# Performance work log

Measured on AMD Instinct MI355X. Metric: run time of the kernel, lower is better.

Reference implementation:

```python
import jax, jax.numpy as jnp
import numpy as np
import math

NUM_HEADS = 12
POS_BND = 16                 # patch_num
RPE_NUM = 2 * POS_BND + 1    # 33
LOGIT_SCALE_MAX = math.log(1.0 / 0.01)
EPS_NORM = 1e-12


def setup_inputs() -> dict:
    key = jax.random.key(0)
    ks = jax.random.split(key, 8)
    L, N, C = 257, 32, 768   # L = 16*16 patches + 1 CLS
    H, W = 16, 16
    x = jax.random.normal(ks[0], (L, N, C), dtype=jnp.float32)
    depth = jax.random.uniform(ks[1], (N, 1, H, W), dtype=jnp.float32)
    in_proj_w = jax.random.normal(ks[2], (3 * C, C), dtype=jnp.float32) * 0.02
    in_proj_b = jnp.zeros((3 * C,), dtype=jnp.float32)
    out_proj_w = jax.random.normal(ks[3], (C, C), dtype=jnp.float32) * 0.02
    out_proj_b = jnp.zeros((C,), dtype=jnp.float32)
    rpe_table = jax.random.normal(ks[4], (3 * RPE_NUM, NUM_HEADS), dtype=jnp.float32) * 0.02
    logit_scale = jnp.log(10.0) * jnp.ones((NUM_HEADS, 1, 1), dtype=jnp.float32)
    return {
        "x": x, "depth": depth,
        "in_proj_w": in_proj_w, "in_proj_b": in_proj_b,
        "out_proj_w": out_proj_w, "out_proj_b": out_proj_b,
        "rpe_table": rpe_table, "logit_scale": logit_scale,
    }


def _rpe_bias(depth, rpe_table):
    # depth: (B, 1, H, W) -> bias (B*num_heads, H*W, H*W)
    d = depth[:, 0]                              # (B, H, W)
    B, H, W = d.shape
    ii, jj = jnp.meshgrid(jnp.arange(H), jnp.arange(W), indexing="ij")
    xg = (jj.astype(jnp.float32) / (W - 1))[None].repeat(B, axis=0)   # (B,H,W)
    yg = (ii.astype(jnp.float32) / (H - 1))[None].repeat(B, axis=0)
    z_min = d.min(axis=(-2, -1), keepdims=True)
    z_max = d.max(axis=(-2, -1), keepdims=True)
    z = (d - z_min) / (z_max - z_min + 1e-8)
    coords = jnp.stack([xg, yg, z], axis=-1).reshape(B, H * W, 3)     # (B,HW,3)
    rel = coords[:, :, None, :] - coords[:, None, :, :]               # (B,HW,HW,3)
    idx = jnp.clip(jnp.round(rel * POS_BND).astype(jnp.int32), -POS_BND, POS_BND)
    idx = idx + POS_BND + jnp.arange(3, dtype=jnp.int32) * RPE_NUM    # (B,HW,HW,3)
    bias = rpe_table[idx].sum(axis=3)                                 # (B,HW,HW,heads)
    bias = bias.transpose(0, 3, 1, 2)                                 # (B,heads,HW,HW)
    return bias.reshape(-1, H * W, H * W)


def reference(x, depth, in_proj_w, in_proj_b, out_proj_w, out_proj_b, rpe_table, logit_scale):
    L, N, C = x.shape
    Hn = NUM_HEADS
    hd = C // Hn
    qkv = x @ in_proj_w.T + in_proj_b                     # (L,N,3C)
    q, k, v = jnp.split(qkv, 3, axis=-1)
    def to_heads(t):
        return t.reshape(L, N * Hn, hd).transpose(1, 0, 2)  # (N*Hn, L, hd)
    q, k, v = to_heads(q), to_heads(k), to_heads(v)
    # scaled-cosine attention: normalized q,k then clamped exp(log-scale)
    qn = q / jnp.maximum(jnp.linalg.norm(q, axis=-1, keepdims=True), EPS_NORM)
    kn = k / jnp.maximum(jnp.linalg.norm(k, axis=-1, keepdims=True), EPS_NORM)
    attn = jnp.einsum("bld,bmd->blm", qn, kn)             # (N*Hn, L, L)
    scale = jnp.exp(jnp.minimum(logit_scale, LOGIT_SCALE_MAX))   # (Hn,1,1)
    attn = (attn.reshape(N, Hn, L, L) * scale).reshape(N * Hn, L, L)
    # relative-position bias on patch tokens (skip CLS at index 0)
    res = _rpe_bias(depth, rpe_table)                     # (N*Hn, L-1, L-1)
    attn = attn.at[:, 1:, 1:].add(res)
    attn = jax.nn.softmax(attn, axis=-1)
    out = jnp.einsum("blm,bmd->bld", attn, v)             # (N*Hn, L, hd)
    out = out.transpose(1, 0, 2).reshape(L, N, C)
    out = out @ out_proj_w.T + out_proj_b
    return out, attn
```

## Files before the change

kernel.cpp:

```cpp
#include <hip/hip_runtime.h>
#include <math.h>

#define L_TOK 257
#define N_B 32
#define C_DIM 768
#define N_H 12
#define HD 64
#define BH (N_B * N_H)
#define M_TOK (L_TOK * N_B)
#define HW 256
#define RPE_NUM 33
#define LOGIT_MAX 4.6051701859880913680f
#define VT_STRIDE 264
#define MT_Q 65
#define NT_Q 18
#define NT_O 6
#define NTK 24

typedef unsigned short ushort;
typedef unsigned int uint;
typedef __attribute__((ext_vector_type(8))) short short8;
typedef __attribute__((ext_vector_type(4))) float f32x4;

__device__ __forceinline__ ushort f2bf_rn(float f) {
  uint u = __float_as_uint(f);
  uint r = (u + 0x7FFF + ((u >> 16) & 1)) >> 16;
  return (ushort)r;
}
__device__ __forceinline__ float bf2f(ushort h) {
  return __uint_as_float(((uint)h) << 16);
}

__device__ __forceinline__ int xcd_swz(int wid, int nwg) {
  int q = nwg >> 3, r = nwg & 7;
  int xcd = wid & 7, pos = wid >> 3;
  int base = (xcd < r) ? xcd * (q + 1) : r * (q + 1) + (xcd - r) * q;
  return base + pos;
}

__device__ __forceinline__ void tile_map(int bid, int MT, int NT, int nwg,
                                         int& m0, int& nt) {
  int wid = xcd_swz(bid, nwg);
  int per = 8 * NT;
  int s = wid / per;
  int rem = wid - s * per;
  int msz = MT - s * 8; if (msz > 8) msz = 8;
  int mi = rem % msz, ni = rem / msz;
  m0 = (s * 8 + mi) * 128;
  nt = ni;
}

__global__ __launch_bounds__(256)
void cvt_split(const float* __restrict__ src, ushort* __restrict__ hi,
               ushort* __restrict__ lo, int n) {
  int i = (blockIdx.x * 256 + threadIdx.x) * 4;
  if (i + 3 >= n + 3) return;
  if (i + 3 < n) {
    float4 v = *(const float4*)(src + i);
    ushort h0 = f2bf_rn(v.x), h1 = f2bf_rn(v.y), h2 = f2bf_rn(v.z), h3 = f2bf_rn(v.w);
    ushort l0 = f2bf_rn(v.x - bf2f(h0)), l1 = f2bf_rn(v.y - bf2f(h1));
    ushort l2 = f2bf_rn(v.z - bf2f(h2)), l3 = f2bf_rn(v.w - bf2f(h3));
    *(ushort4*)(hi + i) = make_ushort4(h0, h1, h2, h3);
    *(ushort4*)(lo + i) = make_ushort4(l0, l1, l2, l3);
  } else {
    for (int k = i; k < n; ++k) {
      float vv = src[k];
      ushort h = f2bf_rn(vv);
      hi[k] = h; lo[k] = f2bf_rn(vv - bf2f(h));
    }
  }
}

__device__ __forceinline__ void stage_pair(const ushort* g0, const ushort* g1,
                                           ushort* l, uint so) {
  __builtin_amdgcn_global_load_lds(
      (const __attribute__((address_space(1))) void*)g0,
      (__attribute__((address_space(3))) void*)((char*)l + so), 16, 0, 0);
  __builtin_amdgcn_global_load_lds(
      (const __attribute__((address_space(1))) void*)g1,
      (__attribute__((address_space(3))) void*)((char*)l + so + 4096), 16, 0, 0);
}

#define PH_WAIT(N)                                        \
  asm volatile("s_waitcnt vmcnt(" #N ")" ::: "memory");   \
  __builtin_amdgcn_s_barrier();                           \
  __builtin_amdgcn_sched_barrier(0);

#define PH_LGKM()                                         \
  asm volatile("s_waitcnt lgkmcnt(0)" ::: "memory");      \
  __builtin_amdgcn_sched_barrier(0);

__device__ __forceinline__ void gemm3_core(
    const ushort* __restrict__ Ahi, const ushort* __restrict__ Alo,
    const ushort* __restrict__ Bhi, const ushort* __restrict__ Blo,
    int m0, int n0, ushort* lds, f32x4 (&acc)[4][4]) {
  const int K = C_DIM, M = M_TOK;
  const int t = threadIdx.x;
  const int wave = t >> 6, lane = t & 63;
  const int wm = (wave & 1) * 64, wn = (wave >> 1) * 64;
  const int frm = lane & 15, fs = lane >> 4;
  const int sx = (fs ^ ((frm >> 1) & 3)) * 8;

  const int ar = t >> 2;
  const int acs = ((t & 3) ^ ((ar >> 1) & 3)) * 8;
  const uint so = (uint)(t & 192) * 16;

  int rA0 = m0 + ar;      if (rA0 > M - 1) rA0 = M - 1;
  int rA1 = m0 + 64 + ar; if (rA1 > M - 1) rA1 = M - 1;
  const size_t gA0 = (size_t)rA0 * K + acs;
  const size_t gA1 = (size_t)rA1 * K + acs;
  const size_t gB0 = (size_t)(n0 + ar) * K + acs;
  const size_t gB1 = (size_t)(n0 + 64 + ar) * K + acs;

  stage_pair(Ahi + gA0, Ahi + gA1, lds, so);
  stage_pair(Bhi + gB0, Bhi + gB1, lds + 4096, so);
  stage_pair(Alo + gA0, Alo + gA1, lds + 8192, so);
  stage_pair(Blo + gB0, Blo + gB1, lds + 12288, so);

  short8 ah[4], bh[4], al[4], bl[4];

#pragma unroll 2
  for (int kt = 0; kt < NTK - 1; ++kt) {
    const int curo = (kt & 1) << 14;
    const int nxo = curo ^ 16384;
    const int kn = (kt + 1) * 32;
    PH_WAIT(4)
#pragma unroll
    for (int i = 0; i < 4; ++i) {
      ah[i] = *(const short8*)(lds + curo + (wm + i * 16 + frm) * 32 + sx);
      bh[i] = *(const short8*)(lds + curo + 4096 + (wn + i * 16 + frm) * 32 + sx);
    }
    stage_pair(Ahi + gA0 + kn, Ahi + gA1 + kn, lds + nxo, so);
    stage_pair(Bhi + gB0 + kn, Bhi + gB1 + kn, lds + nxo + 4096, so);
    PH_LGKM()
    __builtin_amdgcn_s_setprio(1);
#pragma unroll
    for (int i = 0; i < 4; ++i)
#pragma unroll
      for (int j = 0; j < 4; ++j)
        acc[i][j] = __builtin_amdgcn_mfma_f32_16x16x32_bf16(ah[i], bh[j], acc[i][j], 0, 0, 0);
    __builtin_amdgcn_s_setprio(0);
    __builtin_amdgcn_sched_barrier(0);
    PH_WAIT(6)
#pragma unroll
    for (int i = 0; i < 4; ++i)
      al[i] = *(const short8*)(lds + curo + 8192 + (wm + i * 16 + frm) * 32 + sx);
    stage_pair(Alo + gA0 + kn, Alo + gA1 + kn, lds + nxo + 8192, so);
    PH_LGKM()
    __builtin_amdgcn_s_setprio(1);
#pragma unroll
    for (int i = 0; i < 4; ++i)
#pragma unroll
      for (int j = 0; j < 4; ++j)
        acc[i][j] = __builtin_amdgcn_mfma_f32_16x16x32_bf16(al[i], bh[j], acc[i][j], 0, 0, 0);
    __builtin_amdgcn_s_setprio(0);
    __builtin_amdgcn_sched_barrier(0);
    PH_WAIT(6)
#pragma unroll
    for (int i = 0; i < 4; ++i)
      bl[i] = *(const short8*)(lds + curo + 12288 + (wn + i * 16 + frm) * 32 + sx);
    stage_pair(Blo + gB0 + kn, Blo + gB1 + kn, lds + nxo + 12288, so);
    PH_LGKM()
    __builtin_amdgcn_s_setprio(1);
#pragma unroll
    for (int i = 0; i < 4; ++i)
#pragma unroll
      for (int j = 0; j < 4; ++j)
        acc[i][j] = __builtin_amdgcn_mfma_f32_16x16x32_bf16(ah[i], bl[j], acc[i][j], 0, 0, 0);
    __builtin_amdgcn_s_setprio(0);
    __builtin_amdgcn_sched_barrier(0);
  }
  {
    const int curo = ((NTK - 1) & 1) << 14;
    PH_WAIT(4)
#pragma unroll
    for (int i = 0; i < 4; ++i) {
      ah[i] = *(const short8*)(lds + curo + (wm + i * 16 + frm) * 32 + sx);
      bh[i] = *(const short8*)(lds + curo + 4096 + (wn + i * 16 + frm) * 32 + sx);
    }
    PH_LGKM()
#pragma unroll
    for (int i = 0; i < 4; ++i)
#pragma unroll
      for (int j = 0; j < 4; ++j)
        acc[i][j] = __builtin_amdgcn_mfma_f32_16x16x32_bf16(ah[i], bh[j], acc[i][j], 0, 0, 0);
    __builtin_amdgcn_sched_barrier(0);
    PH_WAIT(2)
#pragma unroll
    for (int i = 0; i < 4; ++i)
      al[i] = *(const short8*)(lds + curo + 8192 + (wm + i * 16 + frm) * 32 + sx);
    PH_LGKM()
#pragma unroll
    for (int i = 0; i < 4; ++i)
#pragma unroll
      for (int j = 0; j < 4; ++j)
        acc[i][j] = __builtin_amdgcn_mfma_f32_16x16x32_bf16(al[i], bh[j], acc[i][j], 0, 0, 0);
    __builtin_amdgcn_sched_barrier(0);
    PH_WAIT(0)
#pragma unroll
    for (int i = 0; i < 4; ++i)
      bl[i] = *(const short8*)(lds + curo + 12288 + (wn + i * 16 + frm) * 32 + sx);
    PH_LGKM()
#pragma unroll
    for (int i = 0; i < 4; ++i)
#pragma unroll
      for (int j = 0; j < 4; ++j)
        acc[i][j] = __builtin_amdgcn_mfma_f32_16x16x32_bf16(ah[i], bl[j], acc[i][j], 0, 0, 0);
    __builtin_amdgcn_sched_barrier(0);
  }
}

__global__ __launch_bounds__(256)
void gemm_qkv_fused(const ushort* __restrict__ Ahi, const ushort* __restrict__ Alo,
                    const ushort* __restrict__ Bhi, const ushort* __restrict__ Blo,
                    const float* __restrict__ bias,
                    ushort* __restrict__ qhi, ushort* __restrict__ qlo,
                    ushort* __restrict__ khi, ushort* __restrict__ klo,
                    float* __restrict__ vout) {
  __shared__ __align__(16) ushort lds[32768];
  int m0, nt;
  tile_map(blockIdx.x, MT_Q, NT_Q, MT_Q * NT_Q, m0, nt);
  const int n0 = nt * 128;
  f32x4 acc[4][4] = {};
  gemm3_core(Ahi, Alo, Bhi, Blo, m0, n0, lds, acc);

  const int M = M_TOK;
  const int t = threadIdx.x;
  const int wave = t >> 6, lane = t & 63;
  const int wm = (wave & 1) * 64, wn = (wave >> 1) * 64;
  const int c0 = lane & 15, g = lane >> 4;
  const int colBase = n0 + wn;
  const int sect = colBase / C_DIM;
  const int hh = (colBase - sect * C_DIM) >> 6;
  float bv[4];
#pragma unroll
  for (int j = 0; j < 4; ++j) bv[j] = bias[colBase + j * 16 + c0];

#pragma unroll
  for (int i = 0; i < 4; ++i) {
#pragma unroll
    for (int r = 0; r < 4; ++r) {
      const int row = m0 + wm + i * 16 + g * 4 + r;
      float lv[4];
#pragma unroll
      for (int j = 0; j < 4; ++j) lv[j] = acc[i][j][r] + bv[j];
      if (sect == 2) {
        if (row < M) {
          int l = row >> 5, n = row & 31;
          size_t ob = ((size_t)((n * N_H + hh) * L_TOK + l)) * HD;
#pragma unroll
          for (int j = 0; j < 4; ++j) vout[ob + j * 16 + c0] = lv[j];
        }
      } else {
        float ss = lv[0] * lv[0] + lv[1] * lv[1] + lv[2] * lv[2] + lv[3] * lv[3];
        ss += __shfl_xor(ss, 1);
        ss += __shfl_xor(ss, 2);
        ss += __shfl_xor(ss, 4);
        ss += __shfl_xor(ss, 8);
        float inv = 1.0f / fmaxf(sqrtf(ss), 1e-12f);
        if (row < M) {
          int l = row >> 5, n = row & 31;
          size_t ob = ((size_t)((n * N_H + hh) * L_TOK + l)) * HD;
          ushort* dh = sect ? khi : qhi;
          ushort* dl = sect ? klo : qlo;
#pragma unroll
          for (int j = 0; j < 4; ++j) {
            float val = lv[j] * inv;
            ushort hv = f2bf_rn(val);
            dh[ob + j * 16 + c0] = hv;
            dl[ob + j * 16 + c0] = f2bf_rn(val - bf2f(hv));
          }
        }
      }
    }
  }
}

__global__ __launch_bounds__(256)
void gemm_out(const ushort* __restrict__ Ahi, const ushort* __restrict__ Alo,
              const ushort* __restrict__ Bhi, const ushort* __restrict__ Blo,
              const float* __restrict__ bias, float* __restrict__ Cout) {
  __shared__ __align__(16) ushort lds[32768];
  int m0, nt;
  tile_map(blockIdx.x, MT_Q, NT_O, MT_Q * NT_O, m0, nt);
  const int n0 = nt * 128;
  f32x4 acc[4][4] = {};
  gemm3_core(Ahi, Alo, Bhi, Blo, m0, n0, lds, acc);

  const int M = M_TOK, Nn = C_DIM;
  const int t = threadIdx.x;
  const int wave = t >> 6, lane = t & 63;
  const int wm = (wave & 1) * 64, wn = (wave >> 1) * 64;
  const int ecol = lane & 15;
#pragma unroll
  for (int j = 0; j < 4; ++j) {
    int col = n0 + wn + j * 16 + ecol;
    float bv = bias[col];
#pragma unroll
    for (int i = 0; i < 4; ++i) {
      int rbase = m0 + wm + i * 16 + (lane >> 4) * 4;
#pragma unroll
      for (int r = 0; r < 4; ++r) {
        int row = rbase + r;
        if (row < M) Cout[(size_t)row * Nn + col] = acc[i][j][r] + bv;
      }
    }
  }
}

__global__ __launch_bounds__(256)
void vt_make(const float* __restrict__ v, ushort* __restrict__ vthi,
             ushort* __restrict__ vtlo) {
  __shared__ float sT[64][65];
  const int b = blockIdx.x;
  const int t = threadIdx.x;
  const float* vb = v + (size_t)b * L_TOK * HD;
  ushort* vh = vthi + (size_t)b * HD * VT_STRIDE;
  ushort* vl = vtlo + (size_t)b * HD * VT_STRIDE;
  for (int k0 = 0; k0 < 256; k0 += 64) {
#pragma unroll
    for (int p = 0; p < 16; ++p) {
      int idx = p * 256 + t;
      int k = idx >> 6, d = idx & 63;
      sT[d][k] = vb[(size_t)(k0 + k) * HD + d];
    }
    __syncthreads();
#pragma unroll
    for (int p = 0; p < 16; ++p) {
      int idx = p * 256 + t;
      int d = idx >> 6, k = idx & 63;
      float val = sT[d][k];
      ushort h = f2bf_rn(val);
      vh[(size_t)d * VT_STRIDE + k0 + k] = h;
      vl[(size_t)d * VT_STRIDE + k0 + k] = f2bf_rn(val - bf2f(h));
    }
    __syncthreads();
  }
  if (t < HD) {
    float val = vb[(size_t)256 * HD + t];
    ushort h = f2bf_rn(val);
    vh[(size_t)t * VT_STRIDE + 256] = h;
    vl[(size_t)t * VT_STRIDE + 256] = f2bf_rn(val - bf2f(h));
  }
}

__global__ __launch_bounds__(256)
void attn_mfma(const ushort* __restrict__ qhi, const ushort* __restrict__ qlo,
               const ushort* __restrict__ khi, const ushort* __restrict__ klo,
               const float* __restrict__ depth, const float* __restrict__ rpe,
               const float* __restrict__ lscale, float* __restrict__ P) {
  __shared__ __align__(16) ushort sKh[256 * 72];
  __shared__ __align__(16) ushort sKl[256 * 72];
  __shared__ float cz_s[HW];
  __shared__ float txd[32], tyd[32], tzt[36];
  __shared__ float red_s[16];
  __shared__ float s256[4][16];

  const int tile = blockIdx.x;
  const int b = blockIdx.y;
  const int n = b / N_H, h = b - n * N_H;
  const int t = threadIdx.x;
  const int lane = t & 63, wave = t >> 6;

  float dval = depth[n * HW + t];
  float mn = dval, mx = dval;
#pragma unroll
  for (int o = 32; o > 0; o >>= 1) {
    mn = fminf(mn, __shfl_down(mn, o));
    mx = fmaxf(mx, __shfl_down(mx, o));
  }
  if (lane == 0) { red_s[wave] = mn; red_s[8 + wave] = mx; }
  __syncthreads();
  float zmin = fminf(fminf(red_s[0], red_s[1]), fminf(red_s[2], red_s[3]));
  float zmax = fmaxf(fmaxf(red_s[8], red_s[9]), fmaxf(red_s[10], red_s[11]));
  float den = zmax - zmin + 1e-8f;
  cz_s[t] = (dval - zmin) / den;
  if (t < 31) {
    int d = t - 15;
    int ix = (int)rintf((float)d * (16.0f / 15.0f));
    ix = max(-16, min(16, ix));
    txd[t] = rpe[(ix + 16) * N_H + h];
    tyd[t] = rpe[(RPE_NUM + ix + 16) * N_H + h];
  }
  if (t < RPE_NUM) tzt[t] = rpe[(2 * RPE_NUM + t) * N_H + h];
  const float scale = expf(fminf(lscale[h], LOGIT_MAX));

  const ushort* khb = khi + (size_t)b * L_TOK * HD;
  const ushort* klb = klo + (size_t)b * L_TOK * HD;
#pragma unroll
  for (int it = 0; it < 8; ++it) {
    int idx = it * 256 + t;
    int j = idx >> 3, c = (idx & 7) * 8;
    *(uint4*)(sKh + j * 72 + c) = *(const uint4*)(khb + (size_t)j * HD + c);
    *(uint4*)(sKl + j * 72 + c) = *(const uint4*)(klb + (size_t)j * HD + c);
  }
  __syncthreads();

  const int qrow = tile * 64 + 16 * wave;
  const size_t qoff = ((size_t)b * L_TOK + qrow + (lane & 15)) * HD + (lane >> 4) * 8;
  short8 qh0 = *(const short8*)(qhi + qoff);
  short8 qh1 = *(const short8*)(qhi + qoff + 32);
  short8 ql0 = *(const short8*)(qlo + qoff);
  short8 ql1 = *(const short8*)(qlo + qoff + 32);

  f32x4 acc[16] = {};
#pragma unroll
  for (int jt = 0; jt < 16; ++jt) {
    const ushort* bp = sKh + (jt * 16 + (lane & 15)) * 72 + (lane >> 4) * 8;
    const ushort* bq = sKl + (jt * 16 + (lane & 15)) * 72 + (lane >> 4) * 8;
    short8 bh0 = *(const short8*)(bp);
    short8 bh1 = *(const short8*)(bp + 32);
    short8 bl0 = *(const short8*)(bq);
    short8 bl1 = *(const short8*)(bq + 32);
    acc[jt] = __builtin_amdgcn_mfma_f32_16x16x32_bf16(qh0, bh0, acc[jt], 0, 0, 0);
    acc[jt] = __builtin_amdgcn_mfma_f32_16x16x32_bf16(qh1, bh1, acc[jt], 0, 0, 0);
    acc[jt] = __builtin_amdgcn_mfma_f32_16x16x32_bf16(qh0, bl0, acc[jt], 0, 0, 0);
    acc[jt] = __builtin_amdgcn_mfma_f32_16x16x32_bf16(qh1, bl1, acc[jt], 0, 0, 0);
    acc[jt] = __builtin_amdgcn_mfma_f32_16x16x32_bf16(ql0, bh0, acc[jt], 0, 0, 0);
    acc[jt] = __builtin_amdgcn_mfma_f32_16x16x32_bf16(ql1, bh1, acc[jt], 0, 0, 0);
  }

  {
    const ushort* k6h = khb + (size_t)256 * HD + (lane >> 4) * 8;
    const ushort* k6l = klb + (size_t)256 * HD + (lane >> 4) * 8;
    float p = 0.f;
#pragma unroll
    for (int j = 0; j < 8; ++j) {
      float kf0 = bf2f(k6h[j]) + bf2f(k6l[j]);
      float kf1 = bf2f(k6h[32 + j]) + bf2f(k6l[32 + j]);
      float qf0 = bf2f((ushort)qh0[j]) + bf2f((ushort)ql0[j]);
      float qf1 = bf2f((ushort)qh1[j]) + bf2f((ushort)ql1[j]);
      p = fmaf(qf0, kf0, fmaf(qf1, kf1, p));
    }
    p += __shfl_xor(p, 16);
    p += __shfl_xor(p, 32);
    if (lane < 16) s256[wave][lane] = p;
  }

  const int g = lane >> 4, c0 = lane & 15;

  float lg6[4];
#pragma unroll
  for (int r = 0; r < 4; ++r) {
    int gi = tile * 64 + 16 * wave + 4 * g + r;
    float d6 = s256[wave][4 * g + r];
    float bz = 0.f;
    if (gi >= 1) {
      int dx = ((gi - 1) & 15) - 15;
      int dy = ((gi - 1) >> 4) - 15;
      float rz = (cz_s[gi - 1] - cz_s[255]) * 16.0f;
      int iz = (int)rintf(rz); iz = max(-16, min(16, iz));
      bz = txd[dx + 15] + tyd[dy + 15] + tzt[iz + 16];
    }
    lg6[r] = scale * d6 + bz;
  }

#pragma unroll
  for (int jt = 0; jt < 16; ++jt) {
    int col = jt * 16 + c0;
#pragma unroll
    for (int r = 0; r < 4; ++r) {
      int gi = tile * 64 + 16 * wave + 4 * g + r;
      float lv = scale * acc[jt][r];
      if (col >= 1 && gi >= 1) {
        int dx = ((gi - 1) & 15) - ((col - 1) & 15);
        int dy = ((gi - 1) >> 4) - ((col - 1) >> 4);
        float rz = (cz_s[gi - 1] - cz_s[col - 1]) * 16.0f;
        int iz = (int)rintf(rz); iz = max(-16, min(16, iz));
        lv += txd[dx + 15] + tyd[dy + 15] + tzt[iz + 16];
      }
      acc[jt][r] = lv;
    }
  }

  float* Pb_ = P + (size_t)b * L_TOK * L_TOK;
#pragma unroll
  for (int r = 0; r < 4; ++r) {
    int gi = tile * 64 + 16 * wave + 4 * g + r;
    float m = acc[0][r];
#pragma unroll
    for (int jt = 1; jt < 16; ++jt) m = fmaxf(m, acc[jt][r]);
#pragma unroll
    for (int o = 1; o < 16; o <<= 1) m = fmaxf(m, __shfl_xor(m, o));
    m = fmaxf(m, lg6[r]);
    float s = 0.f;
#pragma unroll
    for (int jt = 0; jt < 16; ++jt) {
      float e = __expf(acc[jt][r] - m);
      acc[jt][r] = e;
      s += e;
    }
#pragma unroll
    for (int o = 1; o < 16; o <<= 1) s += __shfl_xor(s, o);
    float e6 = __expf(lg6[r] - m);
    float inv = 1.0f / (s + e6);
    float* Prow = Pb_ + (size_t)gi * L_TOK;
#pragma unroll
    for (int jt = 0; jt < 16; ++jt)
      Prow[jt * 16 + c0] = acc[jt][r] * inv;
    if (c0 == 0) Prow[256] = e6 * inv;
  }
}

__global__ __launch_bounds__(256)
void attn_row256(const ushort* __restrict__ qhi, const ushort* __restrict__ qlo,
                 const ushort* __restrict__ khi, const ushort* __restrict__ klo,
                 const float* __restrict__ depth, const float* __restrict__ rpe,
                 const float* __restrict__ lscale, float* __restrict__ P) {
  __shared__ float qs[HD];
  __shared__ float cz_s[HW];
  __shared__ float txd[32], tyd[32], tzt[36];
  __shared__ float red_s[16];
  __shared__ float lg6_sh;

  const int b = blockIdx.x;
  const int n = b / N_H, h = b - n * N_H;
  const int t = threadIdx.x;
  const int lane = t & 63, wave = t >> 6;

  float dval = depth[n * HW + t];
  float mn = dval, mx = dval;
#pragma unroll
  for (int o = 32; o > 0; o >>= 1) {
    mn = fminf(mn, __shfl_down(mn, o));
    mx = fmaxf(mx, __shfl_down(mx, o));
  }
  if (lane == 0) { red_s[wave] = mn; red_s[8 + wave] = mx; }
  __syncthreads();
  float zmin = fminf(fminf(red_s[0], red_s[1]), fminf(red_s[2], red_s[3]));
  float zmax = fmaxf(fmaxf(red_s[8], red_s[9]), fmaxf(red_s[10], red_s[11]));
  float den = zmax - zmin + 1e-8f;
  cz_s[t] = (dval - zmin) / den;
  if (t < 31) {
    int d = t - 15;
    int ix = (int)rintf((float)d * (16.0f / 15.0f));
    ix = max(-16, min(16, ix));
    txd[t] = rpe[(ix + 16) * N_H + h];
    tyd[t] = rpe[(RPE_NUM + ix + 16) * N_H + h];
  }
  if (t < RPE_NUM) tzt[t] = rpe[(2 * RPE_NUM + t) * N_H + h];
  const float scale = expf(fminf(lscale[h], LOGIT_MAX));

  const size_t q6 = ((size_t)b * L_TOK + 256) * HD;
  if (t < HD) qs[t] = bf2f(qhi[q6 + t]) + bf2f(qlo[q6 + t]);
  __syncthreads();

  const ushort* krh = khi + ((size_t)b * L_TOK + t) * HD;
  const ushort* krl = klo + ((size_t)b * L_TOK + t) * HD;
  float dot = 0.f;
#pragma unroll
  for (int c = 0; c < HD; c += 8) {
    ushort4 hv0 = *(const ushort4*)(krh + c);
    ushort4 hv1 = *(const ushort4*)(krh + c + 4);
    ushort4 lv0 = *(const ushort4*)(krl + c);
    ushort4 lv1 = *(const ushort4*)(krl + c + 4);
    dot = fmaf(bf2f(hv0.x) + bf2f(lv0.x), qs[c + 0], dot);
    dot = fmaf(bf2f(hv0.y) + bf2f(lv0.y), qs[c + 1], dot);
    dot = fmaf(bf2f(hv0.z) + bf2f(lv0.z), qs[c + 2], dot);
    dot = fmaf(bf2f(hv0.w) + bf2f(lv0.w), qs[c + 3], dot);
    dot = fmaf(bf2f(hv1.x) + bf2f(lv1.x), qs[c + 4], dot);
    dot = fmaf(bf2f(hv1.y) + bf2f(lv1.y), qs[c + 5], dot);
    dot = fmaf(bf2f(hv1.z) + bf2f(lv1.z), qs[c + 6], dot);
    dot = fmaf(bf2f(hv1.w) + bf2f(lv1.w), qs[c + 7], dot);
  }

  float lg;
  {
    float bsum = 0.f;
    if (t >= 1) {
      int dx = 15 - ((t - 1) & 15);
      int dy = 15 - ((t - 1) >> 4);
      float rz = (cz_s[255] - cz_s[t - 1]) * 16.0f;
      int iz = (int)rintf(rz); iz = max(-16, min(16, iz));
      bsum = txd[dx + 15] + tyd[dy + 15] + tzt[iz + 16];
    }
    lg = scale * dot + bsum;
  }

  if (wave == 0) {
    const ushort* k6h = khi + q6;
    const ushort* k6l = klo + q6;
    float pp = (bf2f(k6h[lane]) + bf2f(k6l[lane])) * qs[lane];
#pragma unroll
    for (int o = 32; o > 0; o >>= 1) pp += __shfl_down(pp, o);
    if (lane == 0) {
      float bz = txd[15] + tyd[15] + tzt[16];
      lg6_sh = scale * pp + bz;
    }
  }

  float m = lg;
#pragma unroll
  for (int o = 32; o > 0; o >>= 1) m = fmaxf(m, __shfl_down(m, o));
  if (lane == 0) red_s[wave] = m;
  __syncthreads();
  float M = fmaxf(fmaxf(red_s[0], red_s[1]), fmaxf(red_s[2], red_s[3]));
  M = fmaxf(M, lg6_sh);
  float e = __expf(lg - M);
  float s = e;
#pragma unroll
  for (int o = 32; o > 0; o >>= 1) s += __shfl_down(s, o);
  if (lane == 0) red_s[8 + wave] = s;
  __syncthreads();
  float e6 = __expf(lg6_sh - M);
  float S = (red_s[8] + red_s[9]) + (red_s[10] + red_s[11]) + e6;
  float inv = 1.0f / S;
  float* Prow = P + (size_t)b * L_TOK * L_TOK + (size_t)256 * L_TOK;
  Prow[t] = e * inv;
  if (t == 0) Prow[256] = e6 * inv;
}

__global__ __launch_bounds__(256)
void pv_mfma(const float* __restrict__ P, const ushort* __restrict__ vthi,
             const ushort* __restrict__ vtlo, const float* __restrict__ v,
             ushort* __restrict__ ahi, ushort* __restrict__ alo) {
  const int b = blockIdx.y;
  const int n = b / N_H, h = b - n * N_H;
  const int t = threadIdx.x;
  const int lane = t & 63, wave = t >> 6;
  const int rbase = blockIdx.x * 128 + wave * 32;
  const float* Pb = P + (size_t)b * L_TOK * L_TOK;
  const ushort* vh = vthi + (size_t)b * HD * VT_STRIDE;
  const ushort* vl = vtlo + (size_t)b * HD * VT_STRIDE;

  const int fm = lane & 15, fk = (lane >> 4) * 8;
  f32x4 acc[2][4] = {};

  for (int k0 = 0; k0 < 256; k0 += 32) {
    short8 ah[2], al[2], bh[4], bl[4];
#pragma unroll
    for (int i = 0; i < 2; ++i) {
      const float* pr = Pb + (size_t)(rbase + i * 16 + fm) * L_TOK + k0 + fk;
#pragma unroll
      for (int j = 0; j < 8; ++j) {
        float pv_ = pr[j];
        ushort hh = f2bf_rn(pv_);
        ah[i][j] = (short)hh;
        al[i][j] = (short)f2bf_rn(pv_ - bf2f(hh));
      }
    }
#pragma unroll
    for (int j = 0; j < 4; ++j) {
      const ushort* bp = vh + (size_t)(j * 16 + fm) * VT_STRIDE + k0 + fk;
      const ushort* bq = vl + (size_t)(j * 16 + fm) * VT_STRIDE + k0 + fk;
      bh[j] = *(const short8*)bp;
      bl[j] = *(const short8*)bq;
    }
#pragma unroll
    for (int i = 0; i < 2; ++i)
#pragma unroll
      for (int j = 0; j < 4; ++j) {
        acc[i][j] = __builtin_amdgcn_mfma_f32_16x16x32_bf16(ah[i], bh[j], acc[i][j], 0, 0, 0);
        acc[i][j] = __builtin_amdgcn_mfma_f32_16x16x32_bf16(ah[i], bl[j], acc[i][j], 0, 0, 0);
        acc[i][j] = __builtin_amdgcn_mfma_f32_16x16x32_bf16(al[i], bh[j], acc[i][j], 0, 0, 0);
        acc[i][j] = __builtin_amdgcn_mfma_f32_16x16x32_bf16(al[i], bl[j], acc[i][j], 0, 0, 0);
      }
  }

  const int g = lane >> 4;
  float v6[4];
#pragma unroll
  for (int j = 0; j < 4; ++j)
    v6[j] = v[((size_t)b * L_TOK + 256) * HD + j * 16 + fm];
#pragma unroll
  for (int i = 0; i < 2; ++i)
#pragma unroll
    for (int r = 0; r < 4; ++r) {
      int row = rbase + i * 16 + g * 4 + r;
      float p6 = Pb[(size_t)row * L_TOK + 256];
#pragma unroll
      for (int j = 0; j < 4; ++j) acc[i][j][r] += p6 * v6[j];
    }

#pragma unroll
  for (int i = 0; i < 2; ++i)
#pragma unroll
    for (int r = 0; r < 4; ++r) {
      int row = rbase + i * 16 + g * 4 + r;
      size_t o = ((size_t)row * N_B + n) * C_DIM + h * HD;
#pragma unroll
      for (int j = 0; j < 4; ++j) {
        float val = acc[i][j][r];
        ushort hv = f2bf_rn(val);
        ahi[o + j * 16 + fm] = hv;
        alo[o + j * 16 + fm] = f2bf_rn(val - bf2f(hv));
      }
    }

  if (blockIdx.x == 0 && t < HD) {
    const float* Prow = Pb + (size_t)256 * L_TOK;
    const float* vb = v + (size_t)b * L_TOK * HD;
    float sum = 0.f;
    for (int k = 0; k < L_TOK; ++k)
      sum = fmaf(Prow[k], vb[(size_t)k * HD + t], sum);
    size_t o = ((size_t)256 * N_B + n) * C_DIM + h * HD + t;
    ushort hv = f2bf_rn(sum);
    ahi[o] = hv;
    alo[o] = f2bf_rn(sum - bf2f(hv));
  }
}

extern "C" void kernel_launch(void* const* d_in, const int* in_sizes, int n_in,
                              void* d_out, int out_size, void* d_ws, size_t ws_size,
                              hipStream_t stream) {
  const float* x      = (const float*)d_in[0];
  const float* depth  = (const float*)d_in[1];
  const float* w_in   = (const float*)d_in[2];
  const float* b_in   = (const float*)d_in[3];
  const float* w_out  = (const float*)d_in[4];
  const float* b_out  = (const float*)d_in[5];
  const float* rpe    = (const float*)d_in[6];
  const float* lscale = (const float*)d_in[7];
  float* out = (float*)d_out;
  float* ws = (float*)d_ws;

  ushort* xhi  = (ushort*)ws;
  ushort* xlo  = xhi + 6316032;
  ushort* vthi = (ushort*)(ws + 6316032);
  ushort* vtlo = vthi + 6488064;
  float*  v    = ws + 18948096;
  ushort* qhi  = (ushort*)(ws + 25264128);
  ushort* qlo  = qhi + 6316032;
  ushort* khi  = qlo + 6316032;
  ushort* klo  = khi + 6316032;
  ushort* wihi = (ushort*)(ws + 37896192);
  ushort* wilo = wihi + 1769472;
  ushort* wohi = wilo + 1769472;
  ushort* wolo = wohi + 589824;
  ushort* ahi  = xhi;
  ushort* alo  = xlo;
  float* Pout = out + 6316032;

  cvt_split<<<6168, 256, 0, stream>>>(x, xhi, xlo, 6316032);
  cvt_split<<<1728, 256, 0, stream>>>(w_in, wihi, wilo, 1769472);
  cvt_split<<<576, 256, 0, stream>>>(w_out, wohi, wolo, 589824);

  gemm_qkv_fused<<<MT_Q * NT_Q, 256, 0, stream>>>(xhi, xlo, wihi, wilo, b_in,
                                                  qhi, qlo, khi, klo, v);
  vt_make<<<BH, 256, 0, stream>>>(v, vthi, vtlo);
  attn_mfma<<<dim3(4, BH), 256, 0, stream>>>(qhi, qlo, khi, klo, depth, rpe, lscale, Pout);
  attn_row256<<<BH, 256, 0, stream>>>(qhi, qlo, khi, klo, depth, rpe, lscale, Pout);
  pv_mfma<<<dim3(2, BH), 256, 0, stream>>>(Pout, vthi, vtlo, v, ahi, alo);

  gemm_out<<<MT_Q * NT_O, 256, 0, stream>>>(ahi, alo, wohi, wolo, b_out, out);
}
```

Baseline: 454.3 us.

## Fold last-row attention into attn_mfma, merge lo-fragment loads, add occupancy hints

```diff
diff --git a/kernel.cpp b/kernel.cpp
--- a/kernel.cpp
+++ b/kernel.cpp
@@ -141,27 +141,21 @@
         acc[i][j] = __builtin_amdgcn_mfma_f32_16x16x32_bf16(ah[i], bh[j], acc[i][j], 0, 0, 0);
     __builtin_amdgcn_s_setprio(0);
     __builtin_amdgcn_sched_barrier(0);
-    PH_WAIT(6)
-#pragma unroll
-    for (int i = 0; i < 4; ++i)
+    PH_WAIT(4)
+#pragma unroll
+    for (int i = 0; i < 4; ++i) {
       al[i] = *(const short8*)(lds + curo + 8192 + (wm + i * 16 + frm) * 32 + sx);
+      bl[i] = *(const short8*)(lds + curo + 12288 + (wn + i * 16 + frm) * 32 + sx);
+    }
     stage_pair(Alo + gA0 + kn, Alo + gA1 + kn, lds + nxo + 8192, so);
-    PH_LGKM()
-    __builtin_amdgcn_s_setprio(1);
-#pragma unroll
-    for (int i = 0; i < 4; ++i)
-#pragma unroll
-      for (int j = 0; j < 4; ++j)
-        acc[i][j] = __builtin_amdgcn_mfma_f32_16x16x32_bf16(al[i], bh[j], acc[i][j], 0, 0, 0);
-    __builtin_amdgcn_s_setprio(0);
-    __builtin_amdgcn_sched_barrier(0);
-    PH_WAIT(6)
-#pragma unroll
-    for (int i = 0; i < 4; ++i)
-      bl[i] = *(const short8*)(lds + curo + 12288 + (wn + i * 16 + frm) * 32 + sx);
     stage_pair(Blo + gB0 + kn, Blo + gB1 + kn, lds + nxo + 12288, so);
     PH_LGKM()
     __builtin_amdgcn_s_setprio(1);
+#pragma unroll
+    for (int i = 0; i < 4; ++i)
+#pragma unroll
+      for (int j = 0; j < 4; ++j)
+        acc[i][j] = __builtin_amdgcn_mfma_f32_16x16x32_bf16(al[i], bh[j], acc[i][j], 0, 0, 0);
 #pragma unroll
     for (int i = 0; i < 4; ++i)
 #pragma unroll
@@ -185,22 +179,18 @@
       for (int j = 0; j < 4; ++j)
         acc[i][j] = __builtin_amdgcn_mfma_f32_16x16x32_bf16(ah[i], bh[j], acc[i][j], 0, 0, 0);
     __builtin_amdgcn_sched_barrier(0);
-    PH_WAIT(2)
-#pragma unroll
-    for (int i = 0; i < 4; ++i)
+    PH_WAIT(0)
+#pragma unroll
+    for (int i = 0; i < 4; ++i) {
       al[i] = *(const short8*)(lds + curo + 8192 + (wm + i * 16 + frm) * 32 + sx);
+      bl[i] = *(const short8*)(lds + curo + 12288 + (wn + i * 16 + frm) * 32 + sx);
+    }
     PH_LGKM()
 #pragma unroll
     for (int i = 0; i < 4; ++i)
 #pragma unroll
       for (int j = 0; j < 4; ++j)
         acc[i][j] = __builtin_amdgcn_mfma_f32_16x16x32_bf16(al[i], bh[j], acc[i][j], 0, 0, 0);
-    __builtin_amdgcn_sched_barrier(0);
-    PH_WAIT(0)
-#pragma unroll
-    for (int i = 0; i < 4; ++i)
-      bl[i] = *(const short8*)(lds + curo + 12288 + (wn + i * 16 + frm) * 32 + sx);
-    PH_LGKM()
 #pragma unroll
     for (int i = 0; i < 4; ++i)
 #pragma unroll
@@ -210,7 +200,7 @@
   }
 }
 
-__global__ __launch_bounds__(256)
+__global__ __launch_bounds__(256, 2)
 void gemm_qkv_fused(const ushort* __restrict__ Ahi, const ushort* __restrict__ Alo,
                     const ushort* __restrict__ Bhi, const ushort* __restrict__ Blo,
                     const float* __restrict__ bias,
@@ -276,7 +266,7 @@
   }
 }
 
-__global__ __launch_bounds__(256)
+__global__ __launch_bounds__(256, 2)
 void gemm_out(const ushort* __restrict__ Ahi, const ushort* __restrict__ Alo,
               const ushort* __restrict__ Bhi, const ushort* __restrict__ Blo,
               const float* __restrict__ bias, float* __restrict__ Cout) {
@@ -355,6 +345,8 @@
   __shared__ float txd[32], tyd[32], tzt[36];
   __shared__ float red_s[16];
   __shared__ float s256[4][16];
+  __shared__ float qs[HD];
+  __shared__ float lg6_sh;
 
   const int tile = blockIdx.x;
   const int b = blockIdx.y;
@@ -500,114 +492,77 @@
       Prow[jt * 16 + c0] = acc[jt][r] * inv;
     if (c0 == 0) Prow[256] = e6 * inv;
   }
-}
-
-__global__ __launch_bounds__(256)
-void attn_row256(const ushort* __restrict__ qhi, const ushort* __restrict__ qlo,
-                 const ushort* __restrict__ khi, const ushort* __restrict__ klo,
-                 const float* __restrict__ depth, const float* __restrict__ rpe,
-                 const float* __restrict__ lscale, float* __restrict__ P) {
-  __shared__ float qs[HD];
-  __shared__ float cz_s[HW];
-  __shared__ float txd[32], tyd[32], tzt[36];
-  __shared__ float red_s[16];
-  __shared__ float lg6_sh;
-
-  const int b = blockIdx.x;
-  const int n = b / N_H, h = b - n * N_H;
-  const int t = threadIdx.x;
-  const int lane = t & 63, wave = t >> 6;
-
-  float dval = depth[n * HW + t];
-  float mn = dval, mx = dval;
-#pragma unroll
-  for (int o = 32; o > 0; o >>= 1) {
-    mn = fminf(mn, __shfl_down(mn, o));
-    mx = fmaxf(mx, __shfl_down(mx, o));
-  }
-  if (lane == 0) { red_s[wave] = mn; red_s[8 + wave] = mx; }
-  __syncthreads();
-  float zmin = fminf(fminf(red_s[0], red_s[1]), fminf(red_s[2], red_s[3]));
-  float zmax = fmaxf(fmaxf(red_s[8], red_s[9]), fmaxf(red_s[10], red_s[11]));
-  float den = zmax - zmin + 1e-8f;
-  cz_s[t] = (dval - zmin) / den;
-  if (t < 31) {
-    int d = t - 15;
-    int ix = (int)rintf((float)d * (16.0f / 15.0f));
-    ix = max(-16, min(16, ix));
-    txd[t] = rpe[(ix + 16) * N_H + h];
-    tyd[t] = rpe[(RPE_NUM + ix + 16) * N_H + h];
-  }
-  if (t < RPE_NUM) tzt[t] = rpe[(2 * RPE_NUM + t) * N_H + h];
-  const float scale = expf(fminf(lscale[h], LOGIT_MAX));
-
-  const size_t q6 = ((size_t)b * L_TOK + 256) * HD;
-  if (t < HD) qs[t] = bf2f(qhi[q6 + t]) + bf2f(qlo[q6 + t]);
-  __syncthreads();
-
-  const ushort* krh = khi + ((size_t)b * L_TOK + t) * HD;
-  const ushort* krl = klo + ((size_t)b * L_TOK + t) * HD;
-  float dot = 0.f;
-#pragma unroll
-  for (int c = 0; c < HD; c += 8) {
-    ushort4 hv0 = *(const ushort4*)(krh + c);
-    ushort4 hv1 = *(const ushort4*)(krh + c + 4);
-    ushort4 lv0 = *(const ushort4*)(krl + c);
-    ushort4 lv1 = *(const ushort4*)(krl + c + 4);
-    dot = fmaf(bf2f(hv0.x) + bf2f(lv0.x), qs[c + 0], dot);
-    dot = fmaf(bf2f(hv0.y) + bf2f(lv0.y), qs[c + 1], dot);
-    dot = fmaf(bf2f(hv0.z) + bf2f(lv0.z), qs[c + 2], dot);
-    dot = fmaf(bf2f(hv0.w) + bf2f(lv0.w), qs[c + 3], dot);
-    dot = fmaf(bf2f(hv1.x) + bf2f(lv1.x), qs[c + 4], dot);
-    dot = fmaf(bf2f(hv1.y) + bf2f(lv1.y), qs[c + 5], dot);
-    dot = fmaf(bf2f(hv1.z) + bf2f(lv1.z), qs[c + 6], dot);
-    dot = fmaf(bf2f(hv1.w) + bf2f(lv1.w), qs[c + 7], dot);
-  }
-
-  float lg;
-  {
-    float bsum = 0.f;
-    if (t >= 1) {
-      int dx = 15 - ((t - 1) & 15);
-      int dy = 15 - ((t - 1) >> 4);
-      float rz = (cz_s[255] - cz_s[t - 1]) * 16.0f;
-      int iz = (int)rintf(rz); iz = max(-16, min(16, iz));
-      bsum = txd[dx + 15] + tyd[dy + 15] + tzt[iz + 16];
-    }
-    lg = scale * dot + bsum;
-  }
-
-  if (wave == 0) {
-    const ushort* k6h = khi + q6;
-    const ushort* k6l = klo + q6;
-    float pp = (bf2f(k6h[lane]) + bf2f(k6l[lane])) * qs[lane];
-#pragma unroll
-    for (int o = 32; o > 0; o >>= 1) pp += __shfl_down(pp, o);
-    if (lane == 0) {
-      float bz = txd[15] + tyd[15] + tzt[16];
-      lg6_sh = scale * pp + bz;
-    }
-  }
-
-  float m = lg;
-#pragma unroll
-  for (int o = 32; o > 0; o >>= 1) m = fmaxf(m, __shfl_down(m, o));
-  if (lane == 0) red_s[wave] = m;
-  __syncthreads();
-  float M = fmaxf(fmaxf(red_s[0], red_s[1]), fmaxf(red_s[2], red_s[3]));
-  M = fmaxf(M, lg6_sh);
-  float e = __expf(lg - M);
-  float s = e;
-#pragma unroll
-  for (int o = 32; o > 0; o >>= 1) s += __shfl_down(s, o);
-  if (lane == 0) red_s[8 + wave] = s;
-  __syncthreads();
-  float e6 = __expf(lg6_sh - M);
-  float S = (red_s[8] + red_s[9]) + (red_s[10] + red_s[11]) + e6;
-  float inv = 1.0f / S;
-  float* Prow = P + (size_t)b * L_TOK * L_TOK + (size_t)256 * L_TOK;
-  Prow[t] = e * inv;
-  if (t == 0) Prow[256] = e6 * inv;
+
+  if (tile == 0) {
+    __syncthreads();
+    const size_t q6 = ((size_t)b * L_TOK + 256) * HD;
+    if (t < HD) qs[t] = bf2f(qhi[q6 + t]) + bf2f(qlo[q6 + t]);
+    __syncthreads();
+
+    const ushort* krh = sKh + t * 72;
+    const ushort* krl = sKl + t * 72;
+    float dot = 0.f;
+#pragma unroll
+    for (int c = 0; c < HD; c += 8) {
+      ushort4 hv0 = *(const ushort4*)(krh + c);
+      ushort4 hv1 = *(const ushort4*)(krh + c + 4);
+      ushort4 lv0 = *(const ushort4*)(krl + c);
+      ushort4 lv1 = *(const ushort4*)(krl + c + 4);
+      dot = fmaf(bf2f(hv0.x) + bf2f(lv0.x), qs[c + 0], dot);
+      dot = fmaf(bf2f(hv0.y) + bf2f(lv0.y), qs[c + 1], dot);
+      dot = fmaf(bf2f(hv0.z) + bf2f(lv0.z), qs[c + 2], dot);
+      dot = fmaf(bf2f(hv0.w) + bf2f(lv0.w), qs[c + 3], dot);
+      dot = fmaf(bf2f(hv1.x) + bf2f(lv1.x), qs[c + 4], dot);
+      dot = fmaf(bf2f(hv1.y) + bf2f(lv1.y), qs[c + 5], dot);
+      dot = fmaf(bf2f(hv1.z) + bf2f(lv1.z), qs[c + 6], dot);
+      dot = fmaf(bf2f(hv1.w) + bf2f(lv1.w), qs[c + 7], dot);
+    }
+
+    float lg;
+    {
+      float bsum = 0.f;
+      if (t >= 1) {
+        int dx = 15 - ((t - 1) & 15);
+        int dy = 15 - ((t - 1) >> 4);
+        float rz = (cz_s[255] - cz_s[t - 1]) * 16.0f;
+        int iz = (int)rintf(rz); iz = max(-16, min(16, iz));
+        bsum = txd[dx + 15] + tyd[dy + 15] + tzt[iz + 16];
+      }
+      lg = scale * dot + bsum;
+    }
+
+    if (wave == 0) {
+      const ushort* k6h = khi + q6;
+      const ushort* k6l = klo + q6;
+      float pp = (bf2f(k6h[lane]) + bf2f(k6l[lane])) * qs[lane];
+#pragma unroll
+      for (int o = 32; o > 0; o >>= 1) pp += __shfl_down(pp, o);
+      if (lane == 0) {
+        float bz = txd[15] + tyd[15] + tzt[16];
+        lg6_sh = scale * pp + bz;
+      }
+    }
+
+    float m = lg;
+#pragma unroll
+    for (int o = 32; o > 0; o >>= 1) m = fmaxf(m, __shfl_down(m, o));
+    if (lane == 0) red_s[wave] = m;
+    __syncthreads();
+    float M = fmaxf(fmaxf(red_s[0], red_s[1]), fmaxf(red_s[2], red_s[3]));
+    M = fmaxf(M, lg6_sh);
+    float e = __expf(lg - M);
+    float s = e;
+#pragma unroll
+    for (int o = 32; o > 0; o >>= 1) s += __shfl_down(s, o);
+    if (lane == 0) red_s[8 + wave] = s;
+    __syncthreads();
+    float e6 = __expf(lg6_sh - M);
+    float S = (red_s[8] + red_s[9]) + (red_s[10] + red_s[11]) + e6;
+    float inv = 1.0f / S;
+    float* Prow = Pb_ + (size_t)256 * L_TOK;
+    Prow[t] = e * inv;
+    if (t == 0) Prow[256] = e6 * inv;
+  }
 }
 
 __global__ __launch_bounds__(256)
@@ -739,7 +694,6 @@
                                                   qhi, qlo, khi, klo, v);
   vt_make<<<BH, 256, 0, stream>>>(v, vthi, vtlo);
   attn_mfma<<<dim3(4, BH), 256, 0, stream>>>(qhi, qlo, khi, klo, depth, rpe, lscale, Pout);
-  attn_row256<<<BH, 256, 0, stream>>>(qhi, qlo, khi, klo, depth, rpe, lscale, Pout);
   pv_mfma<<<dim3(2, BH), 256, 0, stream>>>(Pout, vthi, vtlo, v, ahi, alo);
 
   gemm_out<<<MT_Q * NT_O, 256, 0, stream>>>(ahi, alo, wohi, wolo, b_out, out);
```

New measurement: 445.9 us. About the same (-1.8%).
